# Kernel optimization log

Measured on AMD Instinct MI355X. Metric: run time of the kernel, lower is better.

The kernel has to match this reference:

```python
import jax, jax.numpy as jnp
import numpy as np
import math

L, B, D, H = 2048, 4, 1024, 16
DK = D // H
DFF = 4 * D
EPS = 1e-5


def setup_inputs() -> dict:
    key = jax.random.key(0)
    ks = jax.random.split(key, 16)
    s = 1.0 / math.sqrt(D)
    sf = 1.0 / math.sqrt(DFF)
    return {
        "x": jax.random.normal(ks[0], (L, B, D), jnp.float32),
        "Wq": jax.random.normal(ks[1], (D, D), jnp.float32) * s,
        "bq": jnp.zeros((D,), jnp.float32),
        "Wk": jax.random.normal(ks[2], (D, D), jnp.float32) * s,
        "bk": jnp.zeros((D,), jnp.float32),
        "Wv": jax.random.normal(ks[3], (D, D), jnp.float32) * s,
        "bv": jnp.zeros((D,), jnp.float32),
        "Wo": jax.random.normal(ks[4], (D, D), jnp.float32) * s,
        "bo": jnp.zeros((D,), jnp.float32),
        "W1": jax.random.normal(ks[5], (D, DFF), jnp.float32) * s,
        "b1": jnp.zeros((DFF,), jnp.float32),
        "W2": jax.random.normal(ks[6], (DFF, D), jnp.float32) * sf,
        "b2": jnp.zeros((D,), jnp.float32),
        "g1": jnp.ones((D,), jnp.float32),
        "be1": jnp.zeros((D,), jnp.float32),
        "g2": jnp.ones((D,), jnp.float32),
        "be2": jnp.zeros((D,), jnp.float32),
    }


def _layer_norm(x, g, b):
    mu = jnp.mean(x, axis=-1, keepdims=True)
    var = jnp.var(x, axis=-1, keepdims=True)
    return (x - mu) * jax.lax.rsqrt(var + EPS) * g + b


def reference(x, Wq, bq, Wk, bk, Wv, bv, Wo, bo, W1, b1, W2, b2, g1, be1, g2, be2):
    # x: (L, B, D)
    q = x @ Wq + bq
    k = x @ Wk + bk
    v = x @ Wv + bv
    # (L,B,H,dk) -> (B,H,L,dk)
    q = q.reshape(L, B, H, DK).transpose(1, 2, 0, 3)
    k = k.reshape(L, B, H, DK).transpose(1, 2, 0, 3)
    v = v.reshape(L, B, H, DK).transpose(1, 2, 0, 3)
    scale = 1.0 / math.sqrt(DK)
    scores = jnp.einsum('bhqd,bhkd->bhqk', q, k) * scale
    w = jax.nn.softmax(scores, axis=-1)
    attn = jnp.einsum('bhqk,bhkd->bhqd', w, v)  # (B,H,L,dk)
    attn = attn.transpose(2, 0, 1, 3).reshape(L, B, D)
    attn_out = attn @ Wo + bo
    x = _layer_norm(x + attn_out, g1, be1)
    h = jax.nn.gelu(x @ W1 + b1, approximate=False)
    ff = h @ W2 + b2
    return _layer_norm(x + ff, g2, be2)
```

## Files before the change

kernel.cpp:

```cpp
#include <hip/hip_runtime.h>

#define L_   2048
#define B_   4
#define D_   1024
#define H_   16
#define DK_  64
#define DFF_ 4096
#define NT_  (L_*B_)

typedef unsigned short u16;
typedef unsigned int   u32;
typedef __bf16 bf16x8 __attribute__((ext_vector_type(8)));
typedef float  f32x4  __attribute__((ext_vector_type(4)));

__device__ __forceinline__ u16 f2bf(float f) {
  u32 u = __float_as_uint(f);
  u += 0x7fffu + ((u >> 16) & 1u);
  return (u16)(u >> 16);
}
__device__ __forceinline__ float bf2f(u32 lo16) {
  return __uint_as_float(lo16 << 16);
}

#define GLDS16(g, l) __builtin_amdgcn_global_load_lds( \
    (const __attribute__((address_space(1))) void*)(g), \
    (__attribute__((address_space(3))) void*)(l), 16, 0, 0)

#define SCQ_ 0.18033688011112042f

__global__ __launch_bounds__(256) void transpose_w_k(
    const float* __restrict__ W, u16* __restrict__ Wt, int K, int N)
{
  __shared__ float tile[32][33];
  int n0 = blockIdx.x * 32, k0 = blockIdx.y * 32;
  int tx = threadIdx.x, ty = threadIdx.y;
#pragma unroll
  for (int i = ty; i < 32; i += 8)
    tile[i][tx] = W[(size_t)(k0 + i) * N + n0 + tx];
  __syncthreads();
#pragma unroll
  for (int i = ty; i < 32; i += 8)
    Wt[(size_t)(n0 + i) * K + k0 + tx] = f2bf(tile[tx][i]);
}

__global__ __launch_bounds__(256) void transpose_w4_k(
    const float* __restrict__ W0, const float* __restrict__ W1,
    const float* __restrict__ W2, const float* __restrict__ W3,
    u16* __restrict__ dst)
{
  __shared__ float tile[32][33];
  int z = blockIdx.z;
  const float* W = (z == 0) ? W0 : (z == 1) ? W1 : (z == 2) ? W2 : W3;
  u16* Wt = dst + (size_t)z * 1048576;
  int n0 = blockIdx.x * 32, k0 = blockIdx.y * 32;
  int tx = threadIdx.x, ty = threadIdx.y;
#pragma unroll
  for (int i = ty; i < 32; i += 8)
    tile[i][tx] = W[(size_t)(k0 + i) * 1024 + n0 + tx];
  __syncthreads();
#pragma unroll
  for (int i = ty; i < 32; i += 8)
    Wt[(size_t)(n0 + i) * 1024 + k0 + tx] = f2bf(tile[tx][i]);
}

__global__ __launch_bounds__(256) void f32_to_bf16_k(
    const float* __restrict__ in, u16* __restrict__ out, int n4)
{
  int i = blockIdx.x * 256 + threadIdx.x;
  if (i >= n4) return;
  float4 v = ((const float4*)in)[i];
  uint2 r;
  r.x = (u32)f2bf(v.x) | ((u32)f2bf(v.y) << 16);
  r.y = (u32)f2bf(v.z) | ((u32)f2bf(v.w) << 16);
  ((uint2*)out)[i] = r;
}

__global__ __launch_bounds__(256) void bias_concat_k(
    const float* __restrict__ bq, const float* __restrict__ bk,
    const float* __restrict__ bv, float* __restrict__ o)
{
  int i = blockIdx.x * 256 + threadIdx.x;
  float v = (i < 1024) ? bq[i] : ((i < 2048) ? bk[i - 1024] : bv[i - 2048]);
  o[i] = v;
}

template<int BN, int EPI>
__global__ __launch_bounds__(512, 2)
void gemm_pipe(const u16* __restrict__ A, const u16* __restrict__ Bt,
               const float* __restrict__ bias, const void* __restrict__ res,
               u16* __restrict__ outb, int M, int N, int K)
{
  constexpr int BM = 256;
  constexpr int NI  = 2 + BN / 128;
  constexpr int NWN = BN / 64;
  constexpr int NWM = 8 / NWN;
  constexpr int MIT = (BM / NWM) / 16;
  constexpr int NPH = MIT / 4;
  constexpr int BUFB = (BM + BN) * 64;
  __shared__ char SM[4 * BUFB];

  const int tid = threadIdx.x;
  const int w = tid >> 6, lane = tid & 63;
  const int l15 = lane & 15, l4 = lane >> 4;
  const int NK = K >> 5;

  const int gx = gridDim.x;
  int nwg = gx * gridDim.y;
  int id = blockIdx.y * gx + blockIdx.x;
  int q = nwg >> 3, r = nwg & 7;
  int xcd = id & 7, idx = id >> 3;
  int wg = (xcd < r ? xcd * (q + 1) : r * (q + 1) + (xcd - r) * q) + idx;
  const int m0 = (wg / gx) * BM, n0 = (wg % gx) * BN;
  const int wm = (w / NWN) * (BM / NWM), wn = (w % NWN) * 64;

  const u16* gsrc[NI];
#pragma unroll
  for (int k = 0; k < NI; ++k) {
    int o = k * 8192 + tid * 16;
    int col8 = (o >> 4) & 3;
    if (o < BM * 64) {
      int rrow = o >> 6;
      gsrc[k] = A + (size_t)(m0 + rrow) * K + col8 * 8;
    } else {
      int br = (o - BM * 64) >> 6;
      gsrc[k] = Bt + (size_t)(n0 + br) * K + col8 * 8;
    }
  }

  auto stage = [&](int t3, int k) {
    const u16* s = (t3 < NK) ? gsrc[k] + (size_t)t3 * 32 : gsrc[k];
    GLDS16(s, SM + (t3 & 3) * BUFB + k * 8192 + w * 1024);
  };

  for (int t3 = 0; t3 < 3; ++t3)
#pragma unroll
    for (int k = 0; k < NI; ++k) stage(t3, k);
  if constexpr (BN == 256) asm volatile("s_waitcnt vmcnt(8)" ::: "memory");
  else                     asm volatile("s_waitcnt vmcnt(6)" ::: "memory");
  asm volatile("s_barrier" ::: "memory");

  f32x4 acc[MIT][4];
#pragma unroll
  for (int i = 0; i < MIT; ++i)
#pragma unroll
    for (int j = 0; j < 4; ++j) acc[i][j] = (f32x4){0.f, 0.f, 0.f, 0.f};

  for (int t = 0; t < NK; ++t) {
    const char* rb = SM + (t & 3) * BUFB;
    bf16x8 bfr[4];
#pragma unroll
    for (int ph = 0; ph < NPH; ++ph) {
      bf16x8 af[4];
#pragma unroll
      for (int mi = 0; mi < 4; ++mi)
        af[mi] = *(const bf16x8*)(rb + (wm + ph * 64 + mi * 16 + l15) * 64 + l4 * 16);
      if (ph == 0) {
#pragma unroll
        for (int nj = 0; nj < 4; ++nj)
          bfr[nj] = *(const bf16x8*)(rb + BM * 64 + (wn + nj * 16 + l15) * 64 + l4 * 16);
      }
      if constexpr (NPH == 2) {
        stage(t + 3, ph * 2 + 0);
        stage(t + 3, ph * 2 + 1);
      } else {
        stage(t + 3, 0); stage(t + 3, 1); stage(t + 3, 2);
      }
      asm volatile("s_barrier" ::: "memory");
      __builtin_amdgcn_s_setprio(1);
#pragma unroll
      for (int mi = 0; mi < 4; ++mi)
#pragma unroll
        for (int nj = 0; nj < 4; ++nj)
          acc[ph * 4 + mi][nj] = __builtin_amdgcn_mfma_f32_16x16x32_bf16(
              af[mi], bfr[nj], acc[ph * 4 + mi][nj], 0, 0, 0);
      __builtin_amdgcn_s_setprio(0);
      if (ph == NPH - 1) {
        if constexpr (BN == 256) asm volatile("s_waitcnt vmcnt(8)" ::: "memory");
        else                     asm volatile("s_waitcnt vmcnt(6)" ::: "memory");
      }
      asm volatile("s_barrier" ::: "memory");
    }
  }
  asm volatile("s_waitcnt vmcnt(0)" ::: "memory");

  const int gm = m0 + wm + l4 * 4;
  const int gn = n0 + wn + l15;
#pragma unroll
  for (int mi = 0; mi < MIT; ++mi) {
#pragma unroll
    for (int nj = 0; nj < 4; ++nj) {
      int col = gn + nj * 16;
      float bv = bias[col];
#pragma unroll
      for (int rr = 0; rr < 4; ++rr) {
        int row = gm + mi * 16 + rr;
        float v = acc[mi][nj][rr] + bv;
        if (EPI == 2) {
          float gv = 0.5f * v * (1.f + erff(v * 0.70710678118654752f));
          outb[(size_t)row * N + col] = f2bf(gv);
        } else if (EPI == 3) {
          int which = col >> 10, c1 = col & 1023;
          int ll = row >> 2, bb = row & 3;
          int hh = c1 >> 6, dd = c1 & 63;
          if (which == 0) v *= SCQ_;
          outb[(size_t)which * 8388608 +
               ((((size_t)(bb * H_ + hh)) * L_ + ll) << 6) + dd] = f2bf(v);
        } else if (EPI == 5) {
          size_t idxo = (size_t)row * N + col;
          outb[idxo] = f2bf(v + ((const float*)res)[idxo]);
        } else {
          size_t idxo = (size_t)row * N + col;
          outb[idxo] = f2bf(v + bf2f(((const u16*)res)[idxo]));
        }
      }
    }
  }
}

__global__ __launch_bounds__(256, 4)
void attn_fwd2(const u16* __restrict__ qp, const u16* __restrict__ kp,
               const u16* __restrict__ vp, u16* __restrict__ op)
{
  __shared__ u16 Ks[64 * 64];
  __shared__ u16 Vt[64 * 64];
  const int tid = threadIdx.x, w = tid >> 6, lane = tid & 63;
  const int l15 = lane & 15, l4 = lane >> 4;
  const int n = blockIdx.x;
  const int bh = (n & 7) | ((n >> 8) << 3);
  const int qi = (n >> 3) & 31;
  const int q0 = qi * 64;
  const u16* qb = qp + (size_t)bh * L_ * DK_;
  const u16* kb = kp + (size_t)bh * L_ * DK_;
  const u16* vb = vp + (size_t)bh * L_ * DK_;

  bf16x8 qf[2];
#pragma unroll
  for (int kk = 0; kk < 2; ++kk)
    qf[kk] = *(const bf16x8*)&qb[(size_t)(q0 + w * 16 + l15) * DK_ + kk * 32 + l4 * 8];

  f32x4 accO[4];
#pragma unroll
  for (int i = 0; i < 4; ++i) accO[i] = (f32x4){0.f, 0.f, 0.f, 0.f};
  float mrun = -1e30f, lsum = 0.f;

  int rho0 = tid >> 3, rho1 = (256 + tid) >> 3, cseg = lane & 7;
  int kv0 = (rho0 & 32) | ((rho0 & 12) << 1) | ((rho0 & 16) >> 2) | (rho0 & 3);
  int kv1 = (rho1 & 32) | ((rho1 & 12) << 1) | ((rho1 & 16) >> 2) | (rho1 & 3);
  const u16* ksrc0 = kb + (size_t)kv0 * DK_ + ((cseg ^ (rho0 & 7)) << 3);
  const u16* ksrc1 = kb + (size_t)kv1 * DK_ + ((cseg ^ (rho1 & 7)) << 3);
  u16* kdst0 = &Ks[(w * 64) * 8];
  u16* kdst1 = &Ks[(256 + w * 64) * 8];

  const int vseg = tid & 7, vkvp = tid >> 3;
  const u16* vsrc = vb + (size_t)(vkvp * 2) * DK_ + vseg * 8;
  u32* vdst[8];
#pragma unroll
  for (int dd2 = 0; dd2 < 4; ++dd2) {
    int d0 = vseg * 8 + dd2 * 2, d1 = d0 + 1;
    vdst[dd2 * 2] = (u32*)((char*)Vt + d0 * 128 +
        ((((vkvp >> 2) ^ (d0 & 7) ^ (d0 >> 3)) << 4) | ((vkvp & 3) << 2)));
    vdst[dd2 * 2 + 1] = (u32*)((char*)Vt + d1 * 128 +
        ((((vkvp >> 2) ^ (d1 & 7) ^ (d1 >> 3)) << 4) | ((vkvp & 3) << 2)));
  }

  for (int t0 = 0; t0 < L_; t0 += 64) {
    __syncthreads();
    GLDS16(ksrc0 + (size_t)t0 * DK_, kdst0);
    GLDS16(ksrc1 + (size_t)t0 * DK_, kdst1);
    {
      const u16* src = vsrc + (size_t)t0 * DK_;
      uint4 a = *(const uint4*)src;
      uint4 b = *(const uint4*)(src + DK_);
#pragma unroll
      for (int dd2 = 0; dd2 < 4; ++dd2) {
        u32 ai = ((const u32*)&a)[dd2], bi = ((const u32*)&b)[dd2];
        *vdst[dd2 * 2]     = (ai & 0xFFFFu) | (bi << 16);
        *vdst[dd2 * 2 + 1] = (ai >> 16) | (bi & 0xFFFF0000u);
      }
    }
    __syncthreads();

    f32x4 s[4];
#pragma unroll
    for (int i = 0; i < 4; ++i) s[i] = (f32x4){0.f, 0.f, 0.f, 0.f};
#pragma unroll
    for (int kk = 0; kk < 2; ++kk) {
#pragma unroll
      for (int nb = 0; nb < 4; ++nb) {
        int row = nb * 16 + l15;
        bf16x8 kf = *(const bf16x8*)((const char*)Ks + row * 128 +
                                     (((kk * 4 + l4) ^ (row & 7)) << 4));
        s[nb] = __builtin_amdgcn_mfma_f32_16x16x32_bf16(kf, qf[kk], s[nb], 0, 0, 0);
      }
    }

    float pm = fmaxf(fmaxf(s[0][0], s[0][1]), s[0][2]);
    pm = fmaxf(fmaxf(pm, s[0][3]), s[1][0]);
    pm = fmaxf(fmaxf(pm, s[1][1]), s[1][2]);
    pm = fmaxf(fmaxf(pm, s[1][3]), s[2][0]);
    pm = fmaxf(fmaxf(pm, s[2][1]), s[2][2]);
    pm = fmaxf(fmaxf(pm, s[2][3]), s[3][0]);
    pm = fmaxf(fmaxf(pm, s[3][1]), s[3][2]);
    pm = fmaxf(pm, s[3][3]);
    pm = fmaxf(pm, __shfl_xor(pm, 16));
    pm = fmaxf(pm, __shfl_xor(pm, 32));

    if (!__all(pm - mrun <= 8.f)) {
      float mn = fmaxf(mrun, pm);
      float alpha = exp2f(mrun - mn);
      mrun = mn;
      lsum *= alpha;
#pragma unroll
      for (int rr = 0; rr < 4; ++rr) {
        float a4 = __shfl(alpha, l4 * 4 + rr);
        accO[0][rr] *= a4; accO[1][rr] *= a4; accO[2][rr] *= a4; accO[3][rr] *= a4;
      }
    }
#pragma unroll
    for (int i = 0; i < 4; ++i)
#pragma unroll
      for (int rr = 0; rr < 4; ++rr) s[i][rr] = exp2f(s[i][rr] - mrun);
    float ps = 0.f;
#pragma unroll
    for (int i = 0; i < 4; ++i)
      ps += (s[i][0] + s[i][1]) + (s[i][2] + s[i][3]);
    ps += __shfl_xor(ps, 16);
    ps += __shfl_xor(ps, 32);
    lsum += ps;

    u32 pk[2][4];
#pragma unroll
    for (int kk = 0; kk < 2; ++kk)
#pragma unroll
      for (int j2 = 0; j2 < 4; ++j2) {
        int nb = kk * 2 + (j2 >> 1);
        int rr = (j2 & 1) * 2;
        u32 rres;
        asm("v_cvt_pk_bf16_f32 %0, %1, %2" : "=v"(rres) : "v"(s[nb][rr]), "v"(s[nb][rr + 1]));
        pk[kk][j2] = rres;
      }

#pragma unroll
    for (int kk = 0; kk < 2; ++kk) {
      bf16x8 pa;
      ((u32*)&pa)[0] = pk[kk][0];
      ((u32*)&pa)[1] = pk[kk][1];
      ((u32*)&pa)[2] = pk[kk][2];
      ((u32*)&pa)[3] = pk[kk][3];
#pragma unroll
      for (int nb2 = 0; nb2 < 4; ++nb2) {
        int drow = nb2 * 16 + l15;
        bf16x8 vf = *(const bf16x8*)((const char*)Vt + drow * 128 +
                                     (((kk * 4 + l4) ^ (drow & 7) ^ (drow >> 3)) << 4));
        accO[nb2] = __builtin_amdgcn_mfma_f32_16x16x32_bf16(pa, vf, accO[nb2], 0, 0, 0);
      }
    }
  }

  float invl = 1.f / lsum;
  const int bb = bh >> 4, hh = bh & 15;
#pragma unroll
  for (int rr = 0; rr < 4; ++rr) {
    float rl = __shfl(invl, l4 * 4 + rr);
    int qg = q0 + w * 16 + l4 * 4 + rr;
    size_t base = ((size_t)qg * B_ + bb) * D_ + hh * 64;
#pragma unroll
    for (int nb2 = 0; nb2 < 4; ++nb2)
      op[base + nb2 * 16 + l15] = f2bf(accO[nb2][rr] * rl);
  }
}

__global__ __launch_bounds__(256) void layernorm_bf_k(
    const u16* __restrict__ y, const float* __restrict__ g, const float* __restrict__ be,
    float* __restrict__ of, u16* __restrict__ ob)
{
  int row = blockIdx.x, tid = threadIdx.x;
  uint2 raw = *(const uint2*)&y[(size_t)row * D_ + tid * 4];
  float v0 = bf2f(raw.x & 0xffffu), v1 = bf2f(raw.x >> 16);
  float v2 = bf2f(raw.y & 0xffffu), v3 = bf2f(raw.y >> 16);
  float s = (v0 + v1) + (v2 + v3);
  float ss = v0 * v0 + v1 * v1 + v2 * v2 + v3 * v3;
#pragma unroll
  for (int msk = 32; msk >= 1; msk >>= 1) {
    s += __shfl_xor(s, msk);
    ss += __shfl_xor(ss, msk);
  }
  __shared__ float rs[4], rss[4];
  if ((tid & 63) == 0) { rs[tid >> 6] = s; rss[tid >> 6] = ss; }
  __syncthreads();
  s = rs[0] + rs[1] + rs[2] + rs[3];
  ss = rss[0] + rss[1] + rss[2] + rss[3];
  float mu = s * (1.f / D_);
  float var = ss * (1.f / D_) - mu * mu;
  float rstd = rsqrtf(var + 1e-5f);
  int c = tid * 4;
  float o0 = (v0 - mu) * rstd * g[c + 0] + be[c + 0];
  float o1 = (v1 - mu) * rstd * g[c + 1] + be[c + 1];
  float o2 = (v2 - mu) * rstd * g[c + 2] + be[c + 2];
  float o3 = (v3 - mu) * rstd * g[c + 3] + be[c + 3];
  if (of) {
    float4 o = {o0, o1, o2, o3};
    *(float4*)&of[(size_t)row * D_ + c] = o;
  }
  if (ob) {
    uint2 r;
    r.x = (u32)f2bf(o0) | ((u32)f2bf(o1) << 16);
    r.y = (u32)f2bf(o2) | ((u32)f2bf(o3) << 16);
    *(uint2*)&ob[(size_t)row * D_ + c] = r;
  }
}

extern "C" void kernel_launch(void* const* d_in, const int* in_sizes, int n_in,
                              void* d_out, int out_size, void* d_ws, size_t ws_size,
                              hipStream_t stream)
{
  const float* x   = (const float*)d_in[0];
  const float* Wq  = (const float*)d_in[1];
  const float* bq  = (const float*)d_in[2];
  const float* Wk  = (const float*)d_in[3];
  const float* bk  = (const float*)d_in[4];
  const float* Wv  = (const float*)d_in[5];
  const float* bv  = (const float*)d_in[6];
  const float* Wo  = (const float*)d_in[7];
  const float* bo  = (const float*)d_in[8];
  const float* W1f = (const float*)d_in[9];
  const float* b1  = (const float*)d_in[10];
  const float* W2f = (const float*)d_in[11];
  const float* b2  = (const float*)d_in[12];
  const float* g1  = (const float*)d_in[13];
  const float* be1 = (const float*)d_in[14];
  const float* g2  = (const float*)d_in[15];
  const float* be2 = (const float*)d_in[16];

  char* ws = (char*)d_ws;
  const size_t MB = 1024 * 1024;
  u16* WqT  = (u16*)(ws + 0 * MB);
  u16* WoT  = (u16*)(ws + 6 * MB);
  u16* W1T  = (u16*)(ws + 8 * MB);
  u16* W2T  = (u16*)(ws + 16 * MB);
  u16* xb   = (u16*)(ws + 24 * MB);
  u16* qp   = (u16*)(ws + 40 * MB);
  u16* astd = (u16*)(ws + 88 * MB);
  u16* yb   = (u16*)(ws + 104 * MB);
  u16* x1b  = (u16*)(ws + 120 * MB);
  u16* hbuf = (u16*)(ws + 136 * MB);
  float* bcat = (float*)(ws + 200 * MB);
  u16* kp = qp + 8388608;
  u16* vp = qp + 16777216;

  dim3 tb(32, 8);
  transpose_w4_k<<<dim3(32, 32, 4), tb, 0, stream>>>(Wq, Wk, Wv, Wo, WqT);
  transpose_w_k<<<dim3(128, 32), tb, 0, stream>>>(W1f, W1T, D_, DFF_);
  transpose_w_k<<<dim3(32, 128), tb, 0, stream>>>(W2f, W2T, DFF_, D_);
  f32_to_bf16_k<<<NT_ * D_ / 4 / 256, 256, 0, stream>>>(x, xb, NT_ * D_ / 4);
  bias_concat_k<<<12, 256, 0, stream>>>(bq, bk, bv, bcat);

  gemm_pipe<128, 3><<<dim3(24, 32), 512, 0, stream>>>(
      xb, WqT, bcat, nullptr, qp, NT_, 3072, D_);

  attn_fwd2<<<2048, 256, 0, stream>>>(qp, kp, vp, astd);

  gemm_pipe<128, 5><<<dim3(8, 32), 512, 0, stream>>>(
      astd, WoT, bo, x, yb, NT_, D_, D_);
  layernorm_bf_k<<<NT_, 256, 0, stream>>>(yb, g1, be1, nullptr, x1b);
  gemm_pipe<256, 2><<<dim3(16, 32), 512, 0, stream>>>(
      x1b, W1T, b1, nullptr, hbuf, NT_, DFF_, D_);
  gemm_pipe<128, 6><<<dim3(8, 32), 512, 0, stream>>>(
      hbuf, W2T, b2, x1b, yb, NT_, D_, DFF_);
  layernorm_bf_k<<<NT_, 256, 0, stream>>>(yb, g2, be2, (float*)d_out, nullptr);
}
```

Before: 500.0 us.

## Process two query tiles per attention block and swizzle GEMM LDS reads

The attention kernel now gives each block 128 query rows in two 64-row groups instead of 64. Each K/V tile staged into shared memory is reused by twice as many MFMAs, which halves the K/V global and LDS traffic per query, and the grid shrinks to 1024 blocks with launch bounds relaxed to 3 blocks per SIMD. The GEMM now XOR-swizzles the 16-byte column chunk on both the global-to-LDS loads and the fragment reads to reduce LDS bank conflicts. The V transpose packing uses byte-permute instructions. In exchange the attention kernel uses more registers, runs at lower occupancy and has fewer blocks to spread across the GPU.

```diff
diff --git a/kernel.cpp b/kernel.cpp
--- a/kernel.cpp
+++ b/kernel.cpp
@@ -117,7 +117,7 @@
 #pragma unroll
   for (int k = 0; k < NI; ++k) {
     int o = k * 8192 + tid * 16;
-    int col8 = (o >> 4) & 3;
+    int col8 = (((o >> 4) ^ (o >> 6)) & 3);
     if (o < BM * 64) {
       int rrow = o >> 6;
       gsrc[k] = A + (size_t)(m0 + rrow) * K + col8 * 8;
@@ -145,6 +145,8 @@
 #pragma unroll
     for (int j = 0; j < 4; ++j) acc[i][j] = (f32x4){0.f, 0.f, 0.f, 0.f};
 
+  const int csw = (l4 ^ (l15 & 3)) * 16;
+
   for (int t = 0; t < NK; ++t) {
     const char* rb = SM + (t & 3) * BUFB;
     bf16x8 bfr[4];
@@ -153,11 +155,11 @@
       bf16x8 af[4];
 #pragma unroll
       for (int mi = 0; mi < 4; ++mi)
-        af[mi] = *(const bf16x8*)(rb + (wm + ph * 64 + mi * 16 + l15) * 64 + l4 * 16);
+        af[mi] = *(const bf16x8*)(rb + (wm + ph * 64 + mi * 16 + l15) * 64 + csw);
       if (ph == 0) {
 #pragma unroll
         for (int nj = 0; nj < 4; ++nj)
-          bfr[nj] = *(const bf16x8*)(rb + BM * 64 + (wn + nj * 16 + l15) * 64 + l4 * 16);
+          bfr[nj] = *(const bf16x8*)(rb + BM * 64 + (wn + nj * 16 + l15) * 64 + csw);
       }
       if constexpr (NPH == 2) {
         stage(t + 3, ph * 2 + 0);
@@ -217,7 +219,7 @@
   }
 }
 
-__global__ __launch_bounds__(256, 4)
+__global__ __launch_bounds__(256, 3)
 void attn_fwd2(const u16* __restrict__ qp, const u16* __restrict__ kp,
                const u16* __restrict__ vp, u16* __restrict__ op)
 {
@@ -226,22 +228,27 @@
   const int tid = threadIdx.x, w = tid >> 6, lane = tid & 63;
   const int l15 = lane & 15, l4 = lane >> 4;
   const int n = blockIdx.x;
-  const int bh = (n & 7) | ((n >> 8) << 3);
-  const int qi = (n >> 3) & 31;
-  const int q0 = qi * 64;
+  const int bh = (n & 7) | ((n >> 7) << 3);
+  const int qi = (n >> 3) & 15;
+  const int q0 = qi * 128;
   const u16* qb = qp + (size_t)bh * L_ * DK_;
   const u16* kb = kp + (size_t)bh * L_ * DK_;
   const u16* vb = vp + (size_t)bh * L_ * DK_;
 
-  bf16x8 qf[2];
-#pragma unroll
-  for (int kk = 0; kk < 2; ++kk)
-    qf[kk] = *(const bf16x8*)&qb[(size_t)(q0 + w * 16 + l15) * DK_ + kk * 32 + l4 * 8];
-
-  f32x4 accO[4];
-#pragma unroll
-  for (int i = 0; i < 4; ++i) accO[i] = (f32x4){0.f, 0.f, 0.f, 0.f};
-  float mrun = -1e30f, lsum = 0.f;
+  bf16x8 qf[2][2];
+#pragma unroll
+  for (int g = 0; g < 2; ++g)
+#pragma unroll
+    for (int kk = 0; kk < 2; ++kk)
+      qf[g][kk] = *(const bf16x8*)&qb[(size_t)(q0 + g * 64 + w * 16 + l15) * DK_ +
+                                      kk * 32 + l4 * 8];
+
+  f32x4 accO[2][4];
+#pragma unroll
+  for (int g = 0; g < 2; ++g)
+#pragma unroll
+    for (int i = 0; i < 4; ++i) accO[g][i] = (f32x4){0.f, 0.f, 0.f, 0.f};
+  float mrun[2] = {-1e30f, -1e30f}, lsum[2] = {0.f, 0.f};
 
   int rho0 = tid >> 3, rho1 = (256 + tid) >> 3, cseg = lane & 7;
   int kv0 = (rho0 & 32) | ((rho0 & 12) << 1) | ((rho0 & 16) >> 2) | (rho0 & 3);
@@ -263,37 +270,8 @@
         ((((vkvp >> 2) ^ (d1 & 7) ^ (d1 >> 3)) << 4) | ((vkvp & 3) << 2)));
   }
 
-  for (int t0 = 0; t0 < L_; t0 += 64) {
-    __syncthreads();
-    GLDS16(ksrc0 + (size_t)t0 * DK_, kdst0);
-    GLDS16(ksrc1 + (size_t)t0 * DK_, kdst1);
-    {
-      const u16* src = vsrc + (size_t)t0 * DK_;
-      uint4 a = *(const uint4*)src;
-      uint4 b = *(const uint4*)(src + DK_);
-#pragma unroll
-      for (int dd2 = 0; dd2 < 4; ++dd2) {
-        u32 ai = ((const u32*)&a)[dd2], bi = ((const u32*)&b)[dd2];
-        *vdst[dd2 * 2]     = (ai & 0xFFFFu) | (bi << 16);
-        *vdst[dd2 * 2 + 1] = (ai >> 16) | (bi & 0xFFFF0000u);
-      }
-    }
-    __syncthreads();
-
-    f32x4 s[4];
-#pragma unroll
-    for (int i = 0; i < 4; ++i) s[i] = (f32x4){0.f, 0.f, 0.f, 0.f};
-#pragma unroll
-    for (int kk = 0; kk < 2; ++kk) {
-#pragma unroll
-      for (int nb = 0; nb < 4; ++nb) {
-        int row = nb * 16 + l15;
-        bf16x8 kf = *(const bf16x8*)((const char*)Ks + row * 128 +
-                                     (((kk * 4 + l4) ^ (row & 7)) << 4));
-        s[nb] = __builtin_amdgcn_mfma_f32_16x16x32_bf16(kf, qf[kk], s[nb], 0, 0, 0);
-      }
-    }
-
+  auto softmax_pack = [&](f32x4 (&s)[4], float& mr, float& ls,
+                          f32x4 (&aO)[4], u32 (&pk)[2][4]) {
     float pm = fmaxf(fmaxf(s[0][0], s[0][1]), s[0][2]);
     pm = fmaxf(fmaxf(pm, s[0][3]), s[1][0]);
     pm = fmaxf(fmaxf(pm, s[1][1]), s[1][2]);
@@ -304,31 +282,28 @@
     pm = fmaxf(pm, s[3][3]);
     pm = fmaxf(pm, __shfl_xor(pm, 16));
     pm = fmaxf(pm, __shfl_xor(pm, 32));
-
-    if (!__all(pm - mrun <= 8.f)) {
-      float mn = fmaxf(mrun, pm);
-      float alpha = exp2f(mrun - mn);
-      mrun = mn;
-      lsum *= alpha;
+    if (!__all(pm - mr <= 8.f)) {
+      float mn = fmaxf(mr, pm);
+      float alpha = exp2f(mr - mn);
+      mr = mn;
+      ls *= alpha;
 #pragma unroll
       for (int rr = 0; rr < 4; ++rr) {
         float a4 = __shfl(alpha, l4 * 4 + rr);
-        accO[0][rr] *= a4; accO[1][rr] *= a4; accO[2][rr] *= a4; accO[3][rr] *= a4;
+        aO[0][rr] *= a4; aO[1][rr] *= a4; aO[2][rr] *= a4; aO[3][rr] *= a4;
       }
     }
 #pragma unroll
     for (int i = 0; i < 4; ++i)
 #pragma unroll
-      for (int rr = 0; rr < 4; ++rr) s[i][rr] = exp2f(s[i][rr] - mrun);
+      for (int rr = 0; rr < 4; ++rr) s[i][rr] = exp2f(s[i][rr] - mr);
     float ps = 0.f;
 #pragma unroll
     for (int i = 0; i < 4; ++i)
       ps += (s[i][0] + s[i][1]) + (s[i][2] + s[i][3]);
     ps += __shfl_xor(ps, 16);
     ps += __shfl_xor(ps, 32);
-    lsum += ps;
-
-    u32 pk[2][4];
+    ls += ps;
 #pragma unroll
     for (int kk = 0; kk < 2; ++kk)
 #pragma unroll
@@ -336,37 +311,82 @@
         int nb = kk * 2 + (j2 >> 1);
         int rr = (j2 & 1) * 2;
         u32 rres;
-        asm("v_cvt_pk_bf16_f32 %0, %1, %2" : "=v"(rres) : "v"(s[nb][rr]), "v"(s[nb][rr + 1]));
+        asm("v_cvt_pk_bf16_f32 %0, %1, %2" : "=v"(rres)
+            : "v"(s[nb][rr]), "v"(s[nb][rr + 1]));
         pk[kk][j2] = rres;
       }
-
+  };
+
+  for (int t0 = 0; t0 < L_; t0 += 64) {
+    __syncthreads();
+    GLDS16(ksrc0 + (size_t)t0 * DK_, kdst0);
+    GLDS16(ksrc1 + (size_t)t0 * DK_, kdst1);
+    {
+      const u16* src = vsrc + (size_t)t0 * DK_;
+      uint4 a = *(const uint4*)src;
+      uint4 b = *(const uint4*)(src + DK_);
+#pragma unroll
+      for (int dd2 = 0; dd2 < 4; ++dd2) {
+        u32 ai = ((const u32*)&a)[dd2], bi = ((const u32*)&b)[dd2];
+        *vdst[dd2 * 2]     = __builtin_amdgcn_perm(bi, ai, 0x05040100u);
+        *vdst[dd2 * 2 + 1] = __builtin_amdgcn_perm(bi, ai, 0x07060302u);
+      }
+    }
+    __syncthreads();
+
+    f32x4 s0[4], s1[4];
+#pragma unroll
+    for (int i = 0; i < 4; ++i) {
+      s0[i] = (f32x4){0.f, 0.f, 0.f, 0.f};
+      s1[i] = (f32x4){0.f, 0.f, 0.f, 0.f};
+    }
 #pragma unroll
     for (int kk = 0; kk < 2; ++kk) {
-      bf16x8 pa;
-      ((u32*)&pa)[0] = pk[kk][0];
-      ((u32*)&pa)[1] = pk[kk][1];
-      ((u32*)&pa)[2] = pk[kk][2];
-      ((u32*)&pa)[3] = pk[kk][3];
+#pragma unroll
+      for (int nb = 0; nb < 4; ++nb) {
+        int row = nb * 16 + l15;
+        bf16x8 kf = *(const bf16x8*)((const char*)Ks + row * 128 +
+                                     (((kk * 4 + l4) ^ (row & 7)) << 4));
+        s0[nb] = __builtin_amdgcn_mfma_f32_16x16x32_bf16(kf, qf[0][kk], s0[nb], 0, 0, 0);
+        s1[nb] = __builtin_amdgcn_mfma_f32_16x16x32_bf16(kf, qf[1][kk], s1[nb], 0, 0, 0);
+      }
+    }
+
+    u32 pk0[2][4], pk1[2][4];
+    softmax_pack(s0, mrun[0], lsum[0], accO[0], pk0);
+    softmax_pack(s1, mrun[1], lsum[1], accO[1], pk1);
+
+#pragma unroll
+    for (int kk = 0; kk < 2; ++kk) {
+      bf16x8 pa0, pa1;
+      ((u32*)&pa0)[0] = pk0[kk][0]; ((u32*)&pa0)[1] = pk0[kk][1];
+      ((u32*)&pa0)[2] = pk0[kk][2]; ((u32*)&pa0)[3] = pk0[kk][3];
+      ((u32*)&pa1)[0] = pk1[kk][0]; ((u32*)&pa1)[1] = pk1[kk][1];
+      ((u32*)&pa1)[2] = pk1[kk][2]; ((u32*)&pa1)[3] = pk1[kk][3];
 #pragma unroll
       for (int nb2 = 0; nb2 < 4; ++nb2) {
         int drow = nb2 * 16 + l15;
         bf16x8 vf = *(const bf16x8*)((const char*)Vt + drow * 128 +
                                      (((kk * 4 + l4) ^ (drow & 7) ^ (drow >> 3)) << 4));
-        accO[nb2] = __builtin_amdgcn_mfma_f32_16x16x32_bf16(pa, vf, accO[nb2], 0, 0, 0);
-      }
-    }
-  }
-
-  float invl = 1.f / lsum;
+        accO[0][nb2] = __builtin_amdgcn_mfma_f32_16x16x32_bf16(pa0, vf, accO[0][nb2], 0, 0, 0);
+        accO[1][nb2] = __builtin_amdgcn_mfma_f32_16x16x32_bf16(pa1, vf, accO[1][nb2], 0, 0, 0);
+      }
+    }
+  }
+
   const int bb = bh >> 4, hh = bh & 15;
 #pragma unroll
-  for (int rr = 0; rr < 4; ++rr) {
-    float rl = __shfl(invl, l4 * 4 + rr);
-    int qg = q0 + w * 16 + l4 * 4 + rr;
-    size_t base = ((size_t)qg * B_ + bb) * D_ + hh * 64;
-#pragma unroll
-    for (int nb2 = 0; nb2 < 4; ++nb2)
-      op[base + nb2 * 16 + l15] = f2bf(accO[nb2][rr] * rl);
+  for (int g = 0; g < 2; ++g) {
+    float invl = 1.f / lsum[g];
+#pragma unroll
+    for (int rr = 0; rr < 4; ++rr) {
+      float rl = __shfl(invl, l4 * 4 + rr);
+      int qg = q0 + g * 64 + w * 16 + l4 * 4 + rr;
+      size_t base = ((size_t)qg * B_ + bb) * D_ + hh * 64;
+#pragma unroll
+      for (int nb2 = 0; nb2 < 4; ++nb2)
+        op[base + nb2 * 16 + l15] = f2bf(accO[g][nb2][rr] * rl);
+    }
   }
 }
 
@@ -458,7 +478,7 @@
   gemm_pipe<128, 3><<<dim3(24, 32), 512, 0, stream>>>(
       xb, WqT, bcat, nullptr, qp, NT_, 3072, D_);
 
-  attn_fwd2<<<2048, 256, 0, stream>>>(qp, kp, vp, astd);
+  attn_fwd2<<<1024, 256, 0, stream>>>(qp, kp, vp, astd);
 
   gemm_pipe<128, 5><<<dim3(8, 32), 512, 0, stream>>>(
       astd, WoT, bo, x, yb, NT_, D_, D_);
```

Result: no change. 494.4 us (-1.1%).
